# Optimization experiments

Measured on AMD Instinct MI355X. Metric: run time of the kernel, lower is better.

The kernel has to match this reference:

```python
import jax, jax.numpy as jnp
import numpy as np

B, N, K, D, OUT = 4, 65536, 16, 8, 8
EPS = 1e-6      # BatchNorm eps from module
SLOPE = 0.2     # LeakyReLU negative slope


def setup_inputs() -> dict:
    key = jax.random.key(0)
    ks = jax.random.split(key, 4)
    coords = jax.random.normal(ks[0], (B, N, 3), jnp.float32)
    features = jax.random.normal(ks[1], (B, D, N, 1), jnp.float32)
    neighbour_indices = jax.random.randint(ks[2], (B, N, K), 0, N)
    conv_w = jax.random.normal(ks[3], (OUT, 10), jnp.float32) * 0.1  # 1x1 Conv2d weight (out,in)
    conv_b = jnp.zeros((OUT,), jnp.float32)
    bn_gamma = jnp.ones((OUT,), jnp.float32)
    bn_beta = jnp.zeros((OUT,), jnp.float32)
    return dict(coords=coords, features=features, neighbour_indices=neighbour_indices,
                conv_w=conv_w, conv_b=conv_b, bn_gamma=bn_gamma, bn_beta=bn_beta)


def _locse(coords, features, neighbour_indices, conv_w, conv_b, bn_gamma, bn_beta):
    # per-batch gather: (B,N,d),(B,N,K) -> (B,N,K,d)
    gather = jax.vmap(lambda x, i: x[i])
    nb_coords = gather(coords, neighbour_indices)                      # (B,N,K,3)
    ext = jnp.broadcast_to(coords[:, :, None, :], nb_coords.shape)     # (B,N,K,3)
    rel_pos = ext - nb_coords
    rel_dist = jnp.sqrt(jnp.sum(rel_pos * rel_pos, -1, keepdims=True))  # (B,N,K,1)
    rf = jnp.concatenate([rel_dist, rel_pos, ext, nb_coords], -1)       # (B,N,K,10)
    # SharedMLP: 1x1 conv + BatchNorm (training stats, biased var) + LeakyReLU(0.2)
    y = jnp.einsum('bnkc,oc->bnko', rf, conv_w) + conv_b                # (B,N,K,OUT)
    mean = jnp.mean(y, (0, 1, 2))
    var = jnp.mean(jnp.square(y - mean), (0, 1, 2))
    y = bn_gamma * (y - mean) * jax.lax.rsqrt(var + EPS) + bn_beta
    y = jnp.where(y >= 0, y, SLOPE * y)
    # neighbour feature gather: features (B,D,N,1) -> (B,N,D) -> (B,N,K,D)
    nf = gather(jnp.squeeze(features, -1).transpose(0, 2, 1), neighbour_indices)
    out = jnp.concatenate([nf, y], -1)                                  # (B,N,K,D+OUT)
    # match torch channel-first layout (B, 2*d, N, K)
    return jnp.moveaxis(out, -1, 1), jnp.moveaxis(y, -1, 1)


def reference(coords, features, neighbour_indices, conv_w, conv_b, bn_gamma, bn_beta):
    return _locse(coords, features, neighbour_indices, conv_w, conv_b, bn_gamma, bn_beta)
```

## Files before the change

### kernel.cpp

```cpp
#include <hip/hip_runtime.h>
#include <cstdint>
#include <cstddef>

typedef float v4f __attribute__((ext_vector_type(4)));
typedef int   v4i __attribute__((ext_vector_type(4)));

namespace {
constexpr int Bn = 4;
constexpr int Nn = 65536;
constexpr int Kn = 16;
constexpr int NK = Nn * Kn;
constexpr int TOTAL = Bn * NK;
constexpr int QPB = NK / 4;
constexpr float COUNT_F = 4194304.0f;
constexpr float EPS = 1e-6f;
constexpr float SLOPE = 0.2f;
constexpr long long OUT0_TOTAL = (long long)Bn * 16 * NK;
}


__global__ __launch_bounds__(256) void prep_kernel(
    const float* __restrict__ coords,
    const float* __restrict__ features,
    float* __restrict__ stats,
    v4f* __restrict__ cpad,
    v4f* __restrict__ tf)
{
    if (blockIdx.x == 0 && threadIdx.x < 16) stats[threadIdx.x] = 0.0f;
    int t = blockIdx.x * blockDim.x + threadIdx.x;
    if (t >= Bn * Nn) return;
    int b = t >> 16;
    int n = t & (Nn - 1);
    const float* c = coords + (size_t)t * 3;
    v4f cv = {c[0], c[1], c[2], 0.0f};
    cpad[t] = cv;
    const float* fb = features + (size_t)b * 8 * Nn + n;
    v4f lo = {fb[0 * Nn], fb[1 * Nn], fb[2 * Nn], fb[3 * Nn]};
    v4f hi = {fb[4 * Nn], fb[5 * Nn], fb[6 * Nn], fb[7 * Nn]};
    tf[2 * t]     = lo;
    tf[2 * t + 1] = hi;
}

__global__ void init_kernel(float* __restrict__ stats) {
    if (threadIdx.x < 16) stats[threadIdx.x] = 0.0f;
}

template <bool PREP>
__global__ __launch_bounds__(256) void reduce_kernel(
    const v4i* __restrict__ nbr4,
    const v4f* __restrict__ cpad,
    const float* __restrict__ coords,
    const float* __restrict__ conv_w,
    const float* __restrict__ conv_b,
    float* __restrict__ stats)
{
    float w[80];
    #pragma unroll
    for (int i = 0; i < 80; i++) w[i] = conv_w[i];
    float bb[8];
    #pragma unroll
    for (int i = 0; i < 8; i++) bb[i] = conv_b[i];

    float s[8], sq[8];
    #pragma unroll
    for (int i = 0; i < 8; i++) { s[i] = 0.0f; sq[i] = 0.0f; }

    int xcd = blockIdx.x & 7;
    int b   = xcd >> 1;
    int wb  = ((blockIdx.x >> 3) << 1) | (xcd & 1);
    int stride = (gridDim.x >> 2) * blockDim.x;
    const float* cb = coords + (size_t)b * Nn * 3;

    for (int ql = wb * blockDim.x + threadIdx.x; ql < QPB; ql += stride) {
        v4i idx = __builtin_nontemporal_load(&nbr4[(b << 18) + ql]);
        int id[4] = {idx.x, idx.y, idx.z, idx.w};
        int n = ql >> 2;
        float ex, ey, ez;
        if (PREP) {
            v4f e = cpad[(b << 16) + n];
            ex = e.x; ey = e.y; ez = e.z;
        } else {
            ex = cb[n * 3]; ey = cb[n * 3 + 1]; ez = cb[n * 3 + 2];
        }
        #pragma unroll
        for (int k = 0; k < 4; k++) {
            float nx, ny, nz;
            if (PREP) {
                v4f q = cpad[(b << 16) + id[k]];
                nx = q.x; ny = q.y; nz = q.z;
            } else {
                nx = cb[id[k] * 3]; ny = cb[id[k] * 3 + 1]; nz = cb[id[k] * 3 + 2];
            }
            float rx = ex - nx, ry = ey - ny, rz = ez - nz;
            float dist = sqrtf(rx * rx + ry * ry + rz * rz);
            float rf[10] = {dist, rx, ry, rz, ex, ey, ez, nx, ny, nz};
            #pragma unroll
            for (int o = 0; o < 8; o++) {
                float y = bb[o];
                #pragma unroll
                for (int c = 0; c < 10; c++) y = fmaf(w[o * 10 + c], rf[c], y);
                s[o] += y;
                sq[o] = fmaf(y, y, sq[o]);
            }
        }
    }

    #pragma unroll
    for (int i = 0; i < 8; i++) {
        #pragma unroll
        for (int off = 32; off > 0; off >>= 1) {
            s[i]  += __shfl_xor(s[i], off, 64);
            sq[i] += __shfl_xor(sq[i], off, 64);
        }
    }
    __shared__ float ls[4][16];
    int lane = threadIdx.x & 63;
    int wv = threadIdx.x >> 6;
    if (lane == 0) {
        #pragma unroll
        for (int i = 0; i < 8; i++) { ls[wv][i] = s[i]; ls[wv][8 + i] = sq[i]; }
    }
    __syncthreads();
    if (threadIdx.x < 16) {
        float a = ls[0][threadIdx.x] + ls[1][threadIdx.x]
                + ls[2][threadIdx.x] + ls[3][threadIdx.x];
        atomicAdd(&stats[threadIdx.x], a);
    }
}

__global__ void finalize_kernel(
    const float* __restrict__ conv_w,
    const float* __restrict__ conv_b,
    const float* __restrict__ gamma,
    const float* __restrict__ beta,
    float* __restrict__ stats)
{
    int j = threadIdx.x;
    if (j >= 88) return;
    int o = (j < 80) ? (j / 10) : (j - 80);
    float mean = stats[o] * (1.0f / COUNT_F);
    float var = stats[8 + o] * (1.0f / COUNT_F) - mean * mean;
    var = fmaxf(var, 0.0f);
    float scale = gamma[o] * rsqrtf(var + EPS);
    if (j < 80) stats[16 + j] = conv_w[j] * scale;
    else        stats[96 + o] = (conv_b[o] - mean) * scale + beta[o];
}

template <bool PREP>
__global__ __launch_bounds__(256) void output_kernel(
    const v4i* __restrict__ nbr4,
    const v4f* __restrict__ cpad,
    const float* __restrict__ coords,
    const v4f* __restrict__ tf,
    const float* __restrict__ features,
    const float* __restrict__ stats,
    float* __restrict__ out)
{
    float w[80];
    #pragma unroll
    for (int i = 0; i < 80; i++) w[i] = stats[16 + i];
    float bb[8];
    #pragma unroll
    for (int i = 0; i < 8; i++) bb[i] = stats[96 + i];

    int xcd = blockIdx.x & 7;
    int b   = xcd >> 1;
    int wb  = ((blockIdx.x >> 3) << 1) | (xcd & 1);
    int ql  = wb * blockDim.x + threadIdx.x;
    int n   = ql >> 2;

    v4i idx = __builtin_nontemporal_load(&nbr4[(b << 18) + ql]);
    int id[4] = {idx.x, idx.y, idx.z, idx.w};

    const float* cb = coords + (size_t)b * Nn * 3;
    float ex, ey, ez;
    if (PREP) {
        v4f e = cpad[(b << 16) + n];
        ex = e.x; ey = e.y; ez = e.z;
    } else {
        ex = cb[n * 3]; ey = cb[n * 3 + 1]; ez = cb[n * 3 + 2];
    }

    float* o0 = out + ((size_t)b << 24) + (size_t)ql * 4;
    float* o1 = out + OUT0_TOTAL + ((size_t)(b * 8) << 20) + (size_t)ql * 4;

    if (PREP) {
        v4f lo[4], hi[4];
        #pragma unroll
        for (int k = 0; k < 4; k++) {
            lo[k] = tf[2 * ((b << 16) + id[k])];
            hi[k] = tf[2 * ((b << 16) + id[k]) + 1];
        }
        #pragma unroll
        for (int c = 0; c < 4; c++) {
            v4f vlo = {lo[0][c], lo[1][c], lo[2][c], lo[3][c]};
            v4f vhi = {hi[0][c], hi[1][c], hi[2][c], hi[3][c]};
            __builtin_nontemporal_store(vlo, (v4f*)(o0 + (size_t)c * NK));
            __builtin_nontemporal_store(vhi, (v4f*)(o0 + (size_t)(4 + c) * NK));
        }
    } else {
        const float* fb = features + (size_t)b * 8 * Nn;
        #pragma unroll
        for (int d = 0; d < 8; d++) {
            v4f v = {fb[(size_t)d * Nn + id[0]], fb[(size_t)d * Nn + id[1]],
                     fb[(size_t)d * Nn + id[2]], fb[(size_t)d * Nn + id[3]]};
            __builtin_nontemporal_store(v, (v4f*)(o0 + (size_t)d * NK));
        }
    }

    float acc[8][4];
    #pragma unroll
    for (int k = 0; k < 4; k++) {
        float nx, ny, nz;
        if (PREP) {
            v4f q = cpad[(b << 16) + id[k]];
            nx = q.x; ny = q.y; nz = q.z;
        } else {
            nx = cb[id[k] * 3]; ny = cb[id[k] * 3 + 1]; nz = cb[id[k] * 3 + 2];
        }
        float rx = ex - nx, ry = ey - ny, rz = ez - nz;
        float dist = sqrtf(rx * rx + ry * ry + rz * rz);
        float rf[10] = {dist, rx, ry, rz, ex, ey, ez, nx, ny, nz};
        #pragma unroll
        for (int o = 0; o < 8; o++) {
            float y = bb[o];
            #pragma unroll
            for (int c = 0; c < 10; c++) y = fmaf(w[o * 10 + c], rf[c], y);
            acc[o][k] = fmaxf(y, SLOPE * y);
        }
    }
    #pragma unroll
    for (int o = 0; o < 8; o++) {
        v4f v = {acc[o][0], acc[o][1], acc[o][2], acc[o][3]};
        __builtin_nontemporal_store(v, (v4f*)(o0 + (size_t)(8 + o) * NK));
        __builtin_nontemporal_store(v, (v4f*)(o1 + (size_t)o * NK));
    }
}

extern "C" void kernel_launch(void* const* d_in, const int* in_sizes, int n_in,
                              void* d_out, int out_size, void* d_ws, size_t ws_size,
                              hipStream_t stream) {
    const float* coords   = (const float*)d_in[0];
    const float* features = (const float*)d_in[1];
    const int*   nbr      = (const int*)d_in[2];
    const float* conv_w   = (const float*)d_in[3];
    const float* conv_b   = (const float*)d_in[4];
    const float* gamma    = (const float*)d_in[5];
    const float* beta     = (const float*)d_in[6];
    float* out = (float*)d_out;
    const v4i* nbr4 = (const v4i*)nbr;

    float* stats = (float*)d_ws;
    const size_t CPAD_OFF = 1024;
    const size_t CPAD_BYTES = (size_t)Bn * Nn * 4 * sizeof(float);
    const size_t TF_OFF = CPAD_OFF + CPAD_BYTES;
    const size_t TF_BYTES = (size_t)Bn * Nn * 8 * sizeof(float);
    const size_t NEED = TF_OFF + TF_BYTES;
    v4f* cpad = (v4f*)((char*)d_ws + CPAD_OFF);
    v4f* tf   = (v4f*)((char*)d_ws + TF_OFF);

    const bool prep = (ws_size >= NEED);
    if (prep) {
        prep_kernel<<<(Bn * Nn) / 256, 256, 0, stream>>>(coords, features, stats, cpad, tf);
        reduce_kernel<true><<<1024, 256, 0, stream>>>(nbr4, cpad, coords, conv_w, conv_b, stats);
    } else {
        init_kernel<<<1, 64, 0, stream>>>(stats);
        reduce_kernel<false><<<1024, 256, 0, stream>>>(nbr4, cpad, coords, conv_w, conv_b, stats);
    }
    finalize_kernel<<<1, 128, 0, stream>>>(conv_w, conv_b, gamma, beta, stats);
    if (prep)
        output_kernel<true><<<4096, 256, 0, stream>>>(nbr4, cpad, coords, tf, features, stats, out);
    else
        output_kernel<false><<<4096, 256, 0, stream>>>(nbr4, cpad, coords, tf, features, stats, out);
}
```

Measured before the change: 475.0 us.

## Fold BN finalize into output kernel, scalarize weights, double reduce grid

Removes the separate finalize kernel launch: every output thread now recomputes the BatchNorm scale and shift from the accumulated stats and folds them into the conv weights. Weights are wrapped in readfirstlane so the compiler can hold them in scalar registers, which eases VGPR pressure. All neighbour gathers (cpad and tf) are issued together before the stores to increase memory-level parallelism. The reduce grid is doubled to 2048 blocks. The cost is redundant per-thread rsqrt work and more atomics in the reduction.

```diff
diff --git a/kernel.cpp b/kernel.cpp
--- a/kernel.cpp
+++ b/kernel.cpp
@@ -16,6 +16,10 @@
 constexpr float EPS = 1e-6f;
 constexpr float SLOPE = 0.2f;
 constexpr long long OUT0_TOTAL = (long long)Bn * 16 * NK;
+}
+
+__device__ __forceinline__ float uni(float x) {
+    return __int_as_float(__builtin_amdgcn_readfirstlane(__float_as_int(x)));
 }
 
 
@@ -56,10 +60,10 @@
 {
     float w[80];
     #pragma unroll
-    for (int i = 0; i < 80; i++) w[i] = conv_w[i];
+    for (int i = 0; i < 80; i++) w[i] = uni(conv_w[i]);
     float bb[8];
     #pragma unroll
-    for (int i = 0; i < 8; i++) bb[i] = conv_b[i];
+    for (int i = 0; i < 8; i++) bb[i] = uni(conv_b[i]);
 
     float s[8], sq[8];
     #pragma unroll
@@ -128,24 +132,6 @@
     }
 }
 
-__global__ void finalize_kernel(
-    const float* __restrict__ conv_w,
-    const float* __restrict__ conv_b,
-    const float* __restrict__ gamma,
-    const float* __restrict__ beta,
-    float* __restrict__ stats)
-{
-    int j = threadIdx.x;
-    if (j >= 88) return;
-    int o = (j < 80) ? (j / 10) : (j - 80);
-    float mean = stats[o] * (1.0f / COUNT_F);
-    float var = stats[8 + o] * (1.0f / COUNT_F) - mean * mean;
-    var = fmaxf(var, 0.0f);
-    float scale = gamma[o] * rsqrtf(var + EPS);
-    if (j < 80) stats[16 + j] = conv_w[j] * scale;
-    else        stats[96 + o] = (conv_b[o] - mean) * scale + beta[o];
-}
-
 template <bool PREP>
 __global__ __launch_bounds__(256) void output_kernel(
     const v4i* __restrict__ nbr4,
@@ -154,14 +140,23 @@
     const v4f* __restrict__ tf,
     const float* __restrict__ features,
     const float* __restrict__ stats,
+    const float* __restrict__ conv_w,
+    const float* __restrict__ conv_b,
+    const float* __restrict__ gamma,
+    const float* __restrict__ beta,
     float* __restrict__ out)
 {
-    float w[80];
-    #pragma unroll
-    for (int i = 0; i < 80; i++) w[i] = stats[16 + i];
-    float bb[8];
-    #pragma unroll
-    for (int i = 0; i < 8; i++) bb[i] = stats[96 + i];
+    float w[80], bb[8];
+    #pragma unroll
+    for (int o = 0; o < 8; o++) {
+        float mean = stats[o] * (1.0f / COUNT_F);
+        float var = stats[8 + o] * (1.0f / COUNT_F) - mean * mean;
+        var = fmaxf(var, 0.0f);
+        float scale = gamma[o] * rsqrtf(var + EPS);
+        bb[o] = uni((conv_b[o] - mean) * scale + beta[o]);
+        #pragma unroll
+        for (int c = 0; c < 10; c++) w[o * 10 + c] = uni(conv_w[o * 10 + c] * scale);
+    }
 
     int xcd = blockIdx.x & 7;
     int b   = xcd >> 1;
@@ -185,9 +180,10 @@
     float* o1 = out + OUT0_TOTAL + ((size_t)(b * 8) << 20) + (size_t)ql * 4;
 
     if (PREP) {
-        v4f lo[4], hi[4];
-        #pragma unroll
-        for (int k = 0; k < 4; k++) {
+        v4f qc[4], lo[4], hi[4];
+        #pragma unroll
+        for (int k = 0; k < 4; k++) {
+            qc[k] = cpad[(b << 16) + id[k]];
             lo[k] = tf[2 * ((b << 16) + id[k])];
             hi[k] = tf[2 * ((b << 16) + id[k]) + 1];
         }
@@ -198,6 +194,26 @@
             __builtin_nontemporal_store(vlo, (v4f*)(o0 + (size_t)c * NK));
             __builtin_nontemporal_store(vhi, (v4f*)(o0 + (size_t)(4 + c) * NK));
         }
+        float acc[8][4];
+        #pragma unroll
+        for (int k = 0; k < 4; k++) {
+            float rx = ex - qc[k].x, ry = ey - qc[k].y, rz = ez - qc[k].z;
+            float dist = sqrtf(rx * rx + ry * ry + rz * rz);
+            float rf[10] = {dist, rx, ry, rz, ex, ey, ez, qc[k].x, qc[k].y, qc[k].z};
+            #pragma unroll
+            for (int o = 0; o < 8; o++) {
+                float y = bb[o];
+                #pragma unroll
+                for (int c = 0; c < 10; c++) y = fmaf(w[o * 10 + c], rf[c], y);
+                acc[o][k] = fmaxf(y, SLOPE * y);
+            }
+        }
+        #pragma unroll
+        for (int o = 0; o < 8; o++) {
+            v4f v = {acc[o][0], acc[o][1], acc[o][2], acc[o][3]};
+            __builtin_nontemporal_store(v, (v4f*)(o0 + (size_t)(8 + o) * NK));
+            __builtin_nontemporal_store(v, (v4f*)(o1 + (size_t)o * NK));
+        }
     } else {
         const float* fb = features + (size_t)b * 8 * Nn;
         #pragma unroll
@@ -206,34 +222,27 @@
                      fb[(size_t)d * Nn + id[2]], fb[(size_t)d * Nn + id[3]]};
             __builtin_nontemporal_store(v, (v4f*)(o0 + (size_t)d * NK));
         }
-    }
-
-    float acc[8][4];
-    #pragma unroll
-    for (int k = 0; k < 4; k++) {
-        float nx, ny, nz;
-        if (PREP) {
-            v4f q = cpad[(b << 16) + id[k]];
-            nx = q.x; ny = q.y; nz = q.z;
-        } else {
-            nx = cb[id[k] * 3]; ny = cb[id[k] * 3 + 1]; nz = cb[id[k] * 3 + 2];
-        }
-        float rx = ex - nx, ry = ey - ny, rz = ez - nz;
-        float dist = sqrtf(rx * rx + ry * ry + rz * rz);
-        float rf[10] = {dist, rx, ry, rz, ex, ey, ez, nx, ny, nz};
+        float acc[8][4];
+        #pragma unroll
+        for (int k = 0; k < 4; k++) {
+            float nx = cb[id[k] * 3], ny = cb[id[k] * 3 + 1], nz = cb[id[k] * 3 + 2];
+            float rx = ex - nx, ry = ey - ny, rz = ez - nz;
+            float dist = sqrtf(rx * rx + ry * ry + rz * rz);
+            float rf[10] = {dist, rx, ry, rz, ex, ey, ez, nx, ny, nz};
+            #pragma unroll
+            for (int o = 0; o < 8; o++) {
+                float y = bb[o];
+                #pragma unroll
+                for (int c = 0; c < 10; c++) y = fmaf(w[o * 10 + c], rf[c], y);
+                acc[o][k] = fmaxf(y, SLOPE * y);
+            }
+        }
         #pragma unroll
         for (int o = 0; o < 8; o++) {
-            float y = bb[o];
-            #pragma unroll
-            for (int c = 0; c < 10; c++) y = fmaf(w[o * 10 + c], rf[c], y);
-            acc[o][k] = fmaxf(y, SLOPE * y);
-        }
-    }
-    #pragma unroll
-    for (int o = 0; o < 8; o++) {
-        v4f v = {acc[o][0], acc[o][1], acc[o][2], acc[o][3]};
-        __builtin_nontemporal_store(v, (v4f*)(o0 + (size_t)(8 + o) * NK));
-        __builtin_nontemporal_store(v, (v4f*)(o1 + (size_t)o * NK));
+            v4f v = {acc[o][0], acc[o][1], acc[o][2], acc[o][3]};
+            __builtin_nontemporal_store(v, (v4f*)(o0 + (size_t)(8 + o) * NK));
+            __builtin_nontemporal_store(v, (v4f*)(o1 + (size_t)o * NK));
+        }
     }
 }
 
@@ -262,14 +271,13 @@
     const bool prep = (ws_size >= NEED);
     if (prep) {
         prep_kernel<<<(Bn * Nn) / 256, 256, 0, stream>>>(coords, features, stats, cpad, tf);
-        reduce_kernel<true><<<1024, 256, 0, stream>>>(nbr4, cpad, coords, conv_w, conv_b, stats);
+        reduce_kernel<true><<<2048, 256, 0, stream>>>(nbr4, cpad, coords, conv_w, conv_b, stats);
+        output_kernel<true><<<4096, 256, 0, stream>>>(nbr4, cpad, coords, tf, features, stats,
+                                                      conv_w, conv_b, gamma, beta, out);
     } else {
         init_kernel<<<1, 64, 0, stream>>>(stats);
-        reduce_kernel<false><<<1024, 256, 0, stream>>>(nbr4, cpad, coords, conv_w, conv_b, stats);
-    }
-    finalize_kernel<<<1, 128, 0, stream>>>(conv_w, conv_b, gamma, beta, stats);
-    if (prep)
-        output_kernel<true><<<4096, 256, 0, stream>>>(nbr4, cpad, coords, tf, features, stats, out);
-    else
-        output_kernel<false><<<4096, 256, 0, stream>>>(nbr4, cpad, coords, tf, features, stats, out);
-}
+        reduce_kernel<false><<<2048, 256, 0, stream>>>(nbr4, cpad, coords, conv_w, conv_b, stats);
+        output_kernel<false><<<4096, 256, 0, stream>>>(nbr4, cpad, coords, tf, features, stats,
+                                                       conv_w, conv_b, gamma, beta, out);
+    }
+}
```

Measured after the change: 487.6 us. 1.03x slower.

## Fuse prep and stats-reduction kernels; one thread per point with batched gathers

Applied to the files above, without the earlier changes.

Merges the prep kernel (padding coords, transposing features) and the BatchNorm statistics reduction into one launch: odd blocks do prep work and even blocks do the reduction. The reduction now assigns one point with all 16 neighbours per thread and issues eight coordinate gathers at a time from the raw coords array, so it no longer waits on the prep output. Stats are zeroed with a memset instead of a separate init kernel. The aim is to remove a launch and a dependency and to raise memory-level parallelism, in exchange for more registers per thread and uncoalesced 3-float gathers.

```diff
diff --git a/kernel.cpp b/kernel.cpp
--- a/kernel.cpp
+++ b/kernel.cpp
@@ -11,7 +11,6 @@
 constexpr int Kn = 16;
 constexpr int NK = Nn * Kn;
 constexpr int TOTAL = Bn * NK;
-constexpr int QPB = NK / 4;
 constexpr float COUNT_F = 4194304.0f;
 constexpr float EPS = 1e-6f;
 constexpr float SLOPE = 0.2f;
@@ -19,84 +18,79 @@
 }
 
 
-__global__ __launch_bounds__(256) void prep_kernel(
+template <bool PREP>
+__global__ __launch_bounds__(256, 4) void prep_reduce_kernel(
     const float* __restrict__ coords,
     const float* __restrict__ features,
+    const v4i*   __restrict__ nbr4,
+    const float* __restrict__ conv_w,
+    const float* __restrict__ conv_b,
     float* __restrict__ stats,
     v4f* __restrict__ cpad,
     v4f* __restrict__ tf)
 {
-    if (blockIdx.x == 0 && threadIdx.x < 16) stats[threadIdx.x] = 0.0f;
-    int t = blockIdx.x * blockDim.x + threadIdx.x;
-    if (t >= Bn * Nn) return;
-    int b = t >> 16;
-    int n = t & (Nn - 1);
-    const float* c = coords + (size_t)t * 3;
-    v4f cv = {c[0], c[1], c[2], 0.0f};
-    cpad[t] = cv;
-    const float* fb = features + (size_t)b * 8 * Nn + n;
-    v4f lo = {fb[0 * Nn], fb[1 * Nn], fb[2 * Nn], fb[3 * Nn]};
-    v4f hi = {fb[4 * Nn], fb[5 * Nn], fb[6 * Nn], fb[7 * Nn]};
-    tf[2 * t]     = lo;
-    tf[2 * t + 1] = hi;
-}
-
-__global__ void init_kernel(float* __restrict__ stats) {
-    if (threadIdx.x < 16) stats[threadIdx.x] = 0.0f;
-}
-
-template <bool PREP>
-__global__ __launch_bounds__(256) void reduce_kernel(
-    const v4i* __restrict__ nbr4,
-    const v4f* __restrict__ cpad,
-    const float* __restrict__ coords,
-    const float* __restrict__ conv_w,
-    const float* __restrict__ conv_b,
-    float* __restrict__ stats)
-{
+    if (blockIdx.x & 1) {
+        if (!PREP) return;
+        int t = (int)(blockIdx.x >> 1) * 256 + threadIdx.x;
+        int b = t >> 16;
+        int n = t & (Nn - 1);
+        const float* c = coords + (size_t)t * 3;
+        v4f cv = {c[0], c[1], c[2], 0.0f};
+        __builtin_nontemporal_store(cv, &cpad[t]);
+        const float* fb = features + (size_t)b * 8 * Nn + n;
+        v4f lo = {fb[0 * Nn], fb[1 * Nn], fb[2 * Nn], fb[3 * Nn]};
+        v4f hi = {fb[4 * Nn], fb[5 * Nn], fb[6 * Nn], fb[7 * Nn]};
+        __builtin_nontemporal_store(lo, &tf[2 * t]);
+        __builtin_nontemporal_store(hi, &tf[2 * t + 1]);
+        return;
+    }
+
     float w[80];
     #pragma unroll
     for (int i = 0; i < 80; i++) w[i] = conv_w[i];
-    float bb[8];
-    #pragma unroll
-    for (int i = 0; i < 8; i++) bb[i] = conv_b[i];
+    float bb8[8];
+    #pragma unroll
+    for (int i = 0; i < 8; i++) bb8[i] = conv_b[i];
+
+    int b = ((int)blockIdx.x & 7) >> 1;
+    int m = (int)blockIdx.x >> 3;
+    int n = m * 256 + (int)threadIdx.x;
+
+    const float* cb = coords + (size_t)b * Nn * 3;
+    float ex = cb[n * 3], ey = cb[n * 3 + 1], ez = cb[n * 3 + 2];
+
+    int id[16];
+    #pragma unroll
+    for (int j = 0; j < 4; j++) {
+        v4i q = __builtin_nontemporal_load(&nbr4[((size_t)b << 18) + (size_t)(n << 2) + j]);
+        id[4 * j]     = q.x;
+        id[4 * j + 1] = q.y;
+        id[4 * j + 2] = q.z;
+        id[4 * j + 3] = q.w;
+    }
 
     float s[8], sq[8];
     #pragma unroll
     for (int i = 0; i < 8; i++) { s[i] = 0.0f; sq[i] = 0.0f; }
 
-    int xcd = blockIdx.x & 7;
-    int b   = xcd >> 1;
-    int wb  = ((blockIdx.x >> 3) << 1) | (xcd & 1);
-    int stride = (gridDim.x >> 2) * blockDim.x;
-    const float* cb = coords + (size_t)b * Nn * 3;
-
-    for (int ql = wb * blockDim.x + threadIdx.x; ql < QPB; ql += stride) {
-        v4i idx = __builtin_nontemporal_load(&nbr4[(b << 18) + ql]);
-        int id[4] = {idx.x, idx.y, idx.z, idx.w};
-        int n = ql >> 2;
-        float ex, ey, ez;
-        if (PREP) {
-            v4f e = cpad[(b << 16) + n];
-            ex = e.x; ey = e.y; ez = e.z;
-        } else {
-            ex = cb[n * 3]; ey = cb[n * 3 + 1]; ez = cb[n * 3 + 2];
-        }
-        #pragma unroll
-        for (int k = 0; k < 4; k++) {
-            float nx, ny, nz;
-            if (PREP) {
-                v4f q = cpad[(b << 16) + id[k]];
-                nx = q.x; ny = q.y; nz = q.z;
-            } else {
-                nx = cb[id[k] * 3]; ny = cb[id[k] * 3 + 1]; nz = cb[id[k] * 3 + 2];
-            }
-            float rx = ex - nx, ry = ey - ny, rz = ez - nz;
+    #pragma unroll
+    for (int h = 0; h < 2; h++) {
+        float px[8], py[8], pz[8];
+        #pragma unroll
+        for (int k = 0; k < 8; k++) {
+            int idx = id[h * 8 + k];
+            px[k] = cb[idx * 3];
+            py[k] = cb[idx * 3 + 1];
+            pz[k] = cb[idx * 3 + 2];
+        }
+        #pragma unroll
+        for (int k = 0; k < 8; k++) {
+            float rx = ex - px[k], ry = ey - py[k], rz = ez - pz[k];
             float dist = sqrtf(rx * rx + ry * ry + rz * rz);
-            float rf[10] = {dist, rx, ry, rz, ex, ey, ez, nx, ny, nz};
+            float rf[10] = {dist, rx, ry, rz, ex, ey, ez, px[k], py[k], pz[k]};
             #pragma unroll
             for (int o = 0; o < 8; o++) {
-                float y = bb[o];
+                float y = bb8[o];
                 #pragma unroll
                 for (int c = 0; c < 10; c++) y = fmaf(w[o * 10 + c], rf[c], y);
                 s[o] += y;
@@ -169,7 +163,7 @@
     int ql  = wb * blockDim.x + threadIdx.x;
     int n   = ql >> 2;
 
-    v4i idx = __builtin_nontemporal_load(&nbr4[(b << 18) + ql]);
+    v4i idx = __builtin_nontemporal_load(&nbr4[((size_t)b << 18) + ql]);
     int id[4] = {idx.x, idx.y, idx.z, idx.w};
 
     const float* cb = coords + (size_t)b * Nn * 3;
@@ -185,9 +179,10 @@
     float* o1 = out + OUT0_TOTAL + ((size_t)(b * 8) << 20) + (size_t)ql * 4;
 
     if (PREP) {
-        v4f lo[4], hi[4];
+        v4f qc[4], lo[4], hi[4];
         #pragma unroll
         for (int k = 0; k < 4; k++) {
+            qc[k] = cpad[(b << 16) + id[k]];
             lo[k] = tf[2 * ((b << 16) + id[k])];
             hi[k] = tf[2 * ((b << 16) + id[k]) + 1];
         }
@@ -198,6 +193,26 @@
             __builtin_nontemporal_store(vlo, (v4f*)(o0 + (size_t)c * NK));
             __builtin_nontemporal_store(vhi, (v4f*)(o0 + (size_t)(4 + c) * NK));
         }
+        float acc[8][4];
+        #pragma unroll
+        for (int k = 0; k < 4; k++) {
+            float rx = ex - qc[k].x, ry = ey - qc[k].y, rz = ez - qc[k].z;
+            float dist = sqrtf(rx * rx + ry * ry + rz * rz);
+            float rf[10] = {dist, rx, ry, rz, ex, ey, ez, qc[k].x, qc[k].y, qc[k].z};
+            #pragma unroll
+            for (int o = 0; o < 8; o++) {
+                float y = bb[o];
+                #pragma unroll
+                for (int c = 0; c < 10; c++) y = fmaf(w[o * 10 + c], rf[c], y);
+                acc[o][k] = fmaxf(y, SLOPE * y);
+            }
+        }
+        #pragma unroll
+        for (int o = 0; o < 8; o++) {
+            v4f v = {acc[o][0], acc[o][1], acc[o][2], acc[o][3]};
+            __builtin_nontemporal_store(v, (v4f*)(o0 + (size_t)(8 + o) * NK));
+            __builtin_nontemporal_store(v, (v4f*)(o1 + (size_t)o * NK));
+        }
     } else {
         const float* fb = features + (size_t)b * 8 * Nn;
         #pragma unroll
@@ -206,34 +221,27 @@
                      fb[(size_t)d * Nn + id[2]], fb[(size_t)d * Nn + id[3]]};
             __builtin_nontemporal_store(v, (v4f*)(o0 + (size_t)d * NK));
         }
-    }
-
-    float acc[8][4];
-    #pragma unroll
-    for (int k = 0; k < 4; k++) {
-        float nx, ny, nz;
-        if (PREP) {
-            v4f q = cpad[(b << 16) + id[k]];
-            nx = q.x; ny = q.y; nz = q.z;
-        } else {
-            nx = cb[id[k] * 3]; ny = cb[id[k] * 3 + 1]; nz = cb[id[k] * 3 + 2];
-        }
-        float rx = ex - nx, ry = ey - ny, rz = ez - nz;
-        float dist = sqrtf(rx * rx + ry * ry + rz * rz);
-        float rf[10] = {dist, rx, ry, rz, ex, ey, ez, nx, ny, nz};
+        float acc[8][4];
+        #pragma unroll
+        for (int k = 0; k < 4; k++) {
+            float nx = cb[id[k] * 3], ny = cb[id[k] * 3 + 1], nz = cb[id[k] * 3 + 2];
+            float rx = ex - nx, ry = ey - ny, rz = ez - nz;
+            float dist = sqrtf(rx * rx + ry * ry + rz * rz);
+            float rf[10] = {dist, rx, ry, rz, ex, ey, ez, nx, ny, nz};
+            #pragma unroll
+            for (int o = 0; o < 8; o++) {
+                float y = bb[o];
+                #pragma unroll
+                for (int c = 0; c < 10; c++) y = fmaf(w[o * 10 + c], rf[c], y);
+                acc[o][k] = fmaxf(y, SLOPE * y);
+            }
+        }
         #pragma unroll
         for (int o = 0; o < 8; o++) {
-            float y = bb[o];
-            #pragma unroll
-            for (int c = 0; c < 10; c++) y = fmaf(w[o * 10 + c], rf[c], y);
-            acc[o][k] = fmaxf(y, SLOPE * y);
-        }
-    }
-    #pragma unroll
-    for (int o = 0; o < 8; o++) {
-        v4f v = {acc[o][0], acc[o][1], acc[o][2], acc[o][3]};
-        __builtin_nontemporal_store(v, (v4f*)(o0 + (size_t)(8 + o) * NK));
-        __builtin_nontemporal_store(v, (v4f*)(o1 + (size_t)o * NK));
+            v4f v = {acc[o][0], acc[o][1], acc[o][2], acc[o][3]};
+            __builtin_nontemporal_store(v, (v4f*)(o0 + (size_t)(8 + o) * NK));
+            __builtin_nontemporal_store(v, (v4f*)(o1 + (size_t)o * NK));
+        }
     }
 }
 
@@ -259,13 +267,15 @@
     v4f* cpad = (v4f*)((char*)d_ws + CPAD_OFF);
     v4f* tf   = (v4f*)((char*)d_ws + TF_OFF);
 
+    hipMemsetAsync(stats, 0, 16 * sizeof(float), stream);
+
     const bool prep = (ws_size >= NEED);
     if (prep) {
-        prep_kernel<<<(Bn * Nn) / 256, 256, 0, stream>>>(coords, features, stats, cpad, tf);
-        reduce_kernel<true><<<1024, 256, 0, stream>>>(nbr4, cpad, coords, conv_w, conv_b, stats);
+        prep_reduce_kernel<true><<<2048, 256, 0, stream>>>(
+            coords, features, nbr4, conv_w, conv_b, stats, cpad, tf);
     } else {
-        init_kernel<<<1, 64, 0, stream>>>(stats);
-        reduce_kernel<false><<<1024, 256, 0, stream>>>(nbr4, cpad, coords, conv_w, conv_b, stats);
+        prep_reduce_kernel<false><<<2048, 256, 0, stream>>>(
+            coords, features, nbr4, conv_w, conv_b, stats, cpad, tf);
     }
     finalize_kernel<<<1, 128, 0, stream>>>(conv_w, conv_b, gamma, beta, stats);
     if (prep)
```

Result: slower. 513.3 us (+8.1%).
